# Performance work log

Hardware: AMD Instinct MI355X
Metric: run time of the kernel (lower is better)

The kernel has to match this reference:

```python
import jax, jax.numpy as jnp
import numpy as np

INPUT_DIM = 512
DIM = 512
N_ACTIONS = 128
BATCH = 2048
SEQ = 128
GN_EPS = 1e-5


def setup_inputs() -> dict:
    key = jax.random.key(0)
    ks = jax.random.split(key, 8)
    precondition = jax.random.normal(ks[0], (BATCH, SEQ, INPUT_DIM), dtype=jnp.float32)
    effect = jax.random.normal(ks[1], (BATCH, SEQ, INPUT_DIM), dtype=jnp.float32)
    action = jax.random.randint(ks[2], (BATCH,), 0, N_ACTIONS)
    # learned params (kaiming-ish scales)
    w_scale = 1.0 / np.sqrt(INPUT_DIM)
    W = jax.random.uniform(ks[3], (N_ACTIONS, DIM, DIM), jnp.float32, -1.0/np.sqrt(DIM), 1.0/np.sqrt(DIM))
    pw = jax.random.uniform(ks[4], (DIM, INPUT_DIM), jnp.float32, -w_scale, w_scale)
    pb = jnp.zeros((DIM,), jnp.float32)
    ew = jax.random.uniform(ks[5], (DIM, INPUT_DIM), jnp.float32, -w_scale, w_scale)
    eb = jnp.zeros((DIM,), jnp.float32)
    gamma = jnp.ones((1,), jnp.float32)
    beta = jnp.zeros((1,), jnp.float32)
    return {"precondition": precondition, "effect": effect, "action": action,
            "W": W, "pw": pw, "pb": pb, "ew": ew, "eb": eb,
            "gamma": gamma, "beta": beta}


def _masked_mean(x):
    # sum over seq divided by per-feature nonzero count: [B,S,F] -> [B,F]
    return x.sum(1) / (x != 0).sum(1).astype(x.dtype)


def _group_norm_1_1(x, gamma, beta):
    # GroupNorm(1,1) on [B,1,F]: normalize each sample over its F features
    m = x.mean(-1, keepdims=True)
    v = ((x - m) ** 2).mean(-1, keepdims=True)
    return gamma[0] * (x - m) * jax.lax.rsqrt(v + GN_EPS) + beta[0]


def reference(precondition, effect, action, W, pw, pb, ew, eb, gamma, beta):
    p_avg = _group_norm_1_1(_masked_mean(precondition), gamma, beta)
    e_avg = _group_norm_1_1(_masked_mean(effect), gamma, beta)
    p_embed = p_avg @ pw.T + pb          # [B, DIM]
    e_embed = e_avg @ ew.T + eb          # [B, DIM]
    # (dropouts are identity in eval mode)
    selected = W[action]                 # gather: [B, DIM, DIM]
    p_transformed = jnp.einsum('bij,bj->bi', selected, p_embed)
    return p_transformed, e_embed
```

## Files before the change

kernel.cpp:

```cpp
#include <hip/hip_runtime.h>

#define BATCH 2048
#define SEQ 128
#define F 512
#define NACT 128
#define GN_EPS 1e-5f

__global__ __launch_bounds__(512) void k_avg_gn(const float* __restrict__ pre,
                                                const float* __restrict__ eff,
                                                const float* __restrict__ gamma,
                                                const float* __restrict__ beta,
                                                float* __restrict__ Np,
                                                float* __restrict__ Ne) {
    const int b = blockIdx.x;
    const int t = blockIdx.y;
    const float* x = (t == 0 ? pre : eff) + (size_t)b * SEQ * F;
    float* dst = (t == 0 ? Np : Ne) + (size_t)b * F;

    __shared__ float psum[4][F];
    __shared__ float pcnt[4][F];
    __shared__ float red[8];
    __shared__ float mv[2];

    const int tid = threadIdx.x;
    const int g = tid >> 7;
    const int fb = (tid & 127) << 2;

    float4 s4 = make_float4(0.f, 0.f, 0.f, 0.f);
    float4 c4 = make_float4(0.f, 0.f, 0.f, 0.f);
    for (int s = g; s < SEQ; s += 4) {
        const float4 v = *reinterpret_cast<const float4*>(x + (size_t)s * F + fb);
        s4.x += v.x; s4.y += v.y; s4.z += v.z; s4.w += v.w;
        c4.x += (v.x != 0.f) ? 1.f : 0.f;
        c4.y += (v.y != 0.f) ? 1.f : 0.f;
        c4.z += (v.z != 0.f) ? 1.f : 0.f;
        c4.w += (v.w != 0.f) ? 1.f : 0.f;
    }
    *reinterpret_cast<float4*>(&psum[g][fb]) = s4;
    *reinterpret_cast<float4*>(&pcnt[g][fb]) = c4;
    __syncthreads();

    const int f = tid;
    float sum = psum[0][f] + psum[1][f] + psum[2][f] + psum[3][f];
    float cnt = pcnt[0][f] + pcnt[1][f] + pcnt[2][f] + pcnt[3][f];
    const float avg = sum / cnt;

    const int lane = tid & 63, wv = tid >> 6;

    float r = avg;
    #pragma unroll
    for (int off = 32; off; off >>= 1) r += __shfl_down(r, off, 64);
    if (lane == 0) red[wv] = r;
    __syncthreads();
    if (tid == 0) {
        float m = 0.f;
        #pragma unroll
        for (int i = 0; i < 8; ++i) m += red[i];
        mv[0] = m * (1.f / F);
    }
    __syncthreads();
    const float m = mv[0];
    const float d = avg - m;

    r = d * d;
    #pragma unroll
    for (int off = 32; off; off >>= 1) r += __shfl_down(r, off, 64);
    if (lane == 0) red[wv] = r;
    __syncthreads();
    if (tid == 0) {
        float v = 0.f;
        #pragma unroll
        for (int i = 0; i < 8; ++i) v += red[i];
        mv[1] = v * (1.f / F);
    }
    __syncthreads();
    const float var = mv[1];
    const float inv = 1.f / sqrtf(var + GN_EPS);

    dst[f] = gamma[0] * d * inv + beta[0];
}

__global__ __launch_bounds__(256) void k_sort(const int* __restrict__ action,
                                              int* __restrict__ sorted,
                                              int* __restrict__ gstart) {
    __shared__ int cnt[NACT];
    __shared__ int start[NACT + 1];
    const int tid = threadIdx.x;
    if (tid < NACT) cnt[tid] = 0;
    __syncthreads();
    for (int b = tid; b < BATCH; b += 256) atomicAdd(&cnt[action[b]], 1);
    __syncthreads();
    if (tid == 0) {
        int acc = 0;
        for (int a = 0; a < NACT; ++a) { start[a] = acc; acc += cnt[a]; }
        start[NACT] = acc;
    }
    __syncthreads();
    if (tid <= NACT) gstart[tid] = start[tid];
    if (tid < NACT) cnt[tid] = start[tid];
    __syncthreads();
    for (int b = tid; b < BATCH; b += 256) {
        const int pos = atomicAdd(&cnt[action[b]], 1);
        sorted[pos] = b;
    }
}

__global__ __launch_bounds__(256) void k_embed(const float* __restrict__ Np,
                                               const float* __restrict__ Ne,
                                               const float* __restrict__ pw,
                                               const float* __restrict__ pb,
                                               const float* __restrict__ ew,
                                               const float* __restrict__ eb,
                                               float* __restrict__ Ep,
                                               float* __restrict__ outE) {
    const int z = blockIdx.z;
    const float* A = z ? Ne : Np;
    const float* Bw = z ? ew : pw;
    const float* bias = z ? eb : pb;
    float* D = z ? outE : Ep;

    const int m0 = blockIdx.x * 64;
    const int n0 = blockIdx.y * 64;

    __shared__ float As[16][68];
    __shared__ float Bs[16][68];

    const int tid = threadIdx.x;
    const int lr = tid >> 2;
    const int lk = (tid & 3) << 2;
    const int tx = tid & 15, ty = tid >> 4;

    float acc[4][4] = {};
    for (int k0 = 0; k0 < F; k0 += 16) {
        const float4 av = *reinterpret_cast<const float4*>(A + (size_t)(m0 + lr) * F + k0 + lk);
        const float4 bv = *reinterpret_cast<const float4*>(Bw + (size_t)(n0 + lr) * F + k0 + lk);
        As[lk + 0][lr] = av.x; As[lk + 1][lr] = av.y; As[lk + 2][lr] = av.z; As[lk + 3][lr] = av.w;
        Bs[lk + 0][lr] = bv.x; Bs[lk + 1][lr] = bv.y; Bs[lk + 2][lr] = bv.z; Bs[lk + 3][lr] = bv.w;
        __syncthreads();
        #pragma unroll
        for (int k = 0; k < 16; ++k) {
            const float4 a = *reinterpret_cast<const float4*>(&As[k][ty * 4]);
            const float4 bq = *reinterpret_cast<const float4*>(&Bs[k][tx * 4]);
            acc[0][0] = fmaf(a.x, bq.x, acc[0][0]); acc[0][1] = fmaf(a.x, bq.y, acc[0][1]);
            acc[0][2] = fmaf(a.x, bq.z, acc[0][2]); acc[0][3] = fmaf(a.x, bq.w, acc[0][3]);
            acc[1][0] = fmaf(a.y, bq.x, acc[1][0]); acc[1][1] = fmaf(a.y, bq.y, acc[1][1]);
            acc[1][2] = fmaf(a.y, bq.z, acc[1][2]); acc[1][3] = fmaf(a.y, bq.w, acc[1][3]);
            acc[2][0] = fmaf(a.z, bq.x, acc[2][0]); acc[2][1] = fmaf(a.z, bq.y, acc[2][1]);
            acc[2][2] = fmaf(a.z, bq.z, acc[2][2]); acc[2][3] = fmaf(a.z, bq.w, acc[2][3]);
            acc[3][0] = fmaf(a.w, bq.x, acc[3][0]); acc[3][1] = fmaf(a.w, bq.y, acc[3][1]);
            acc[3][2] = fmaf(a.w, bq.z, acc[3][2]); acc[3][3] = fmaf(a.w, bq.w, acc[3][3]);
        }
        __syncthreads();
    }

    const float4 b4 = *reinterpret_cast<const float4*>(bias + n0 + tx * 4);
    #pragma unroll
    for (int i = 0; i < 4; ++i) {
        float4 o;
        o.x = acc[i][0] + b4.x;
        o.y = acc[i][1] + b4.y;
        o.z = acc[i][2] + b4.z;
        o.w = acc[i][3] + b4.w;
        *reinterpret_cast<float4*>(D + (size_t)(m0 + ty * 4 + i) * F + n0 + tx * 4) = o;
    }
}

__global__ __launch_bounds__(256) void k_transform(const float* __restrict__ W,
                                                   const float* __restrict__ Ep,
                                                   const int* __restrict__ sorted,
                                                   const int* __restrict__ gstart,
                                                   float* __restrict__ outP) {
    const int a = blockIdx.x;
    const int s0 = gstart[a], s1 = gstart[a + 1];
    if (s0 == s1) return;

    const int rowbase = blockIdx.y * 128 + (threadIdx.x >> 6) * 32;
    const int lane = threadIdx.x & 63;
    const float* Wa = W + (size_t)a * F * F;

    for (int c0 = s0; c0 < s1; c0 += 8) {
        int bb[8];
        float4 e0[8], e1[8];
        #pragma unroll
        for (int q = 0; q < 8; ++q) {
            const int src = (c0 + q < s1) ? (c0 + q) : s0;
            bb[q] = sorted[src];
            const float* er = Ep + (size_t)bb[q] * F + lane * 8;
            e0[q] = *reinterpret_cast<const float4*>(er);
            e1[q] = *reinterpret_cast<const float4*>(er + 4);
        }
        for (int r = 0; r < 32; ++r) {
            const int i = rowbase + r;
            const float* wr = Wa + (size_t)i * F + lane * 8;
            const float4 w0 = *reinterpret_cast<const float4*>(wr);
            const float4 w1 = *reinterpret_cast<const float4*>(wr + 4);
            float p[8];
            #pragma unroll
            for (int q = 0; q < 8; ++q) {
                float s = w0.x * e0[q].x;
                s = fmaf(w0.y, e0[q].y, s);
                s = fmaf(w0.z, e0[q].z, s);
                s = fmaf(w0.w, e0[q].w, s);
                s = fmaf(w1.x, e1[q].x, s);
                s = fmaf(w1.y, e1[q].y, s);
                s = fmaf(w1.z, e1[q].z, s);
                s = fmaf(w1.w, e1[q].w, s);
                p[q] = s;
            }
            #pragma unroll
            for (int q = 0; q < 8; ++q) {
                #pragma unroll
                for (int off = 32; off; off >>= 1) p[q] += __shfl_down(p[q], off, 64);
            }
            if (lane == 0) {
                #pragma unroll
                for (int q = 0; q < 8; ++q)
                    if (c0 + q < s1) outP[(size_t)bb[q] * F + i] = p[q];
            }
        }
    }
}

extern "C" void kernel_launch(void* const* d_in, const int* in_sizes, int n_in,
                              void* d_out, int out_size, void* d_ws, size_t ws_size,
                              hipStream_t stream) {
    const float* pre    = (const float*)d_in[0];
    const float* eff    = (const float*)d_in[1];
    const int*   action = (const int*)d_in[2];
    const float* W      = (const float*)d_in[3];
    const float* pw     = (const float*)d_in[4];
    const float* pb     = (const float*)d_in[5];
    const float* ew     = (const float*)d_in[6];
    const float* eb     = (const float*)d_in[7];
    const float* gamma  = (const float*)d_in[8];
    const float* beta   = (const float*)d_in[9];

    float* out  = (float*)d_out;
    float* outP = out;
    float* outE = out + (size_t)BATCH * F;

    float* Np = (float*)d_ws;
    float* Ne = Np + (size_t)BATCH * F;
    float* Ep = Ne + (size_t)BATCH * F;
    int* sorted = (int*)(Ep + (size_t)BATCH * F);
    int* gstart = sorted + BATCH;

    k_avg_gn<<<dim3(BATCH, 2), 512, 0, stream>>>(pre, eff, gamma, beta, Np, Ne);
    k_sort<<<1, 256, 0, stream>>>(action, sorted, gstart);
    k_embed<<<dim3(2048 / 64, 512 / 64, 2), 256, 0, stream>>>(Np, Ne, pw, pb, ew, eb, Ep, outE);
    k_transform<<<dim3(NACT, 4), 256, 0, stream>>>(W, Ep, sorted, gstart, outP);
}
```

Before: 1.238 ms.

## Fuse averaging, group norm, embedding GEMV and sort into one kernel

Merges the masked-mean/group-norm kernel, the action counting-sort kernel and the tiled embedding GEMM into a single launch. Each block now normalizes its row into shared memory and immediately computes the embedding as a per-thread dot product against pw/ew, and one extra block does the sort. This drops two launches and the round trip of the normalized intermediates through global memory. The trade-off is that the embedding becomes a GEMV per row that rereads the full 512x512 weight matrix in every block, relying on L2 to absorb it. The transform kernel is also split into twice as many row blocks to raise parallelism.

```diff
diff --git a/kernel.cpp b/kernel.cpp
--- a/kernel.cpp
+++ b/kernel.cpp
@@ -6,23 +6,58 @@
 #define NACT 128
 #define GN_EPS 1e-5f
 
-__global__ __launch_bounds__(512) void k_avg_gn(const float* __restrict__ pre,
-                                                const float* __restrict__ eff,
-                                                const float* __restrict__ gamma,
-                                                const float* __restrict__ beta,
-                                                float* __restrict__ Np,
-                                                float* __restrict__ Ne) {
-    const int b = blockIdx.x;
-    const int t = blockIdx.y;
+__global__ __launch_bounds__(512) void k_fused(const float* __restrict__ pre,
+                                               const float* __restrict__ eff,
+                                               const int* __restrict__ action,
+                                               const float* __restrict__ pw,
+                                               const float* __restrict__ pb,
+                                               const float* __restrict__ ew,
+                                               const float* __restrict__ eb,
+                                               const float* __restrict__ gamma,
+                                               const float* __restrict__ beta,
+                                               float* __restrict__ Ep,
+                                               float* __restrict__ outE,
+                                               int* __restrict__ sorted,
+                                               int* __restrict__ gstart) {
+    const int blk = blockIdx.x;
+    const int tid = threadIdx.x;
+
+    if (blk == 2 * BATCH) {
+        __shared__ int cnt[NACT];
+        __shared__ int start[NACT + 1];
+        if (tid < NACT) cnt[tid] = 0;
+        __syncthreads();
+        for (int b = tid; b < BATCH; b += 512) atomicAdd(&cnt[action[b]], 1);
+        __syncthreads();
+        if (tid == 0) {
+            int acc = 0;
+            for (int a = 0; a < NACT; ++a) { start[a] = acc; acc += cnt[a]; }
+            start[NACT] = acc;
+        }
+        __syncthreads();
+        if (tid <= NACT) gstart[tid] = start[tid];
+        if (tid < NACT) cnt[tid] = start[tid];
+        __syncthreads();
+        for (int b = tid; b < BATCH; b += 512) {
+            const int pos = atomicAdd(&cnt[action[b]], 1);
+            sorted[pos] = b;
+        }
+        return;
+    }
+
+    const int b = blk >> 1;
+    const int t = blk & 1;
     const float* x = (t == 0 ? pre : eff) + (size_t)b * SEQ * F;
-    float* dst = (t == 0 ? Np : Ne) + (size_t)b * F;
+    const float* wmat = t == 0 ? pw : ew;
+    const float* bias = t == 0 ? pb : eb;
+    float* dst = (t == 0 ? Ep : outE) + (size_t)b * F;
 
     __shared__ float psum[4][F];
     __shared__ float pcnt[4][F];
+    __shared__ float nvec[F];
     __shared__ float red[8];
     __shared__ float mv[2];
 
-    const int tid = threadIdx.x;
     const int g = tid >> 7;
     const int fb = (tid & 127) << 2;
 
@@ -41,9 +76,9 @@
     __syncthreads();
 
     const int f = tid;
-    float sum = psum[0][f] + psum[1][f] + psum[2][f] + psum[3][f];
-    float cnt = pcnt[0][f] + pcnt[1][f] + pcnt[2][f] + pcnt[3][f];
-    const float avg = sum / cnt;
+    const float sum = psum[0][f] + psum[1][f] + psum[2][f] + psum[3][f];
+    const float cntf = pcnt[0][f] + pcnt[1][f] + pcnt[2][f] + pcnt[3][f];
+    const float avg = sum / cntf;
 
     const int lane = tid & 63, wv = tid >> 6;
 
@@ -74,95 +109,25 @@
         mv[1] = v * (1.f / F);
     }
     __syncthreads();
-    const float var = mv[1];
-    const float inv = 1.f / sqrtf(var + GN_EPS);
-
-    dst[f] = gamma[0] * d * inv + beta[0];
-}
-
-__global__ __launch_bounds__(256) void k_sort(const int* __restrict__ action,
-                                              int* __restrict__ sorted,
-                                              int* __restrict__ gstart) {
-    __shared__ int cnt[NACT];
-    __shared__ int start[NACT + 1];
-    const int tid = threadIdx.x;
-    if (tid < NACT) cnt[tid] = 0;
-    __syncthreads();
-    for (int b = tid; b < BATCH; b += 256) atomicAdd(&cnt[action[b]], 1);
-    __syncthreads();
-    if (tid == 0) {
-        int acc = 0;
-        for (int a = 0; a < NACT; ++a) { start[a] = acc; acc += cnt[a]; }
-        start[NACT] = acc;
-    }
-    __syncthreads();
-    if (tid <= NACT) gstart[tid] = start[tid];
-    if (tid < NACT) cnt[tid] = start[tid];
-    __syncthreads();
-    for (int b = tid; b < BATCH; b += 256) {
-        const int pos = atomicAdd(&cnt[action[b]], 1);
-        sorted[pos] = b;
-    }
-}
-
-__global__ __launch_bounds__(256) void k_embed(const float* __restrict__ Np,
-                                               const float* __restrict__ Ne,
-                                               const float* __restrict__ pw,
-                                               const float* __restrict__ pb,
-                                               const float* __restrict__ ew,
-                                               const float* __restrict__ eb,
-                                               float* __restrict__ Ep,
-                                               float* __restrict__ outE) {
-    const int z = blockIdx.z;
-    const float* A = z ? Ne : Np;
-    const float* Bw = z ? ew : pw;
-    const float* bias = z ? eb : pb;
-    float* D = z ? outE : Ep;
-
-    const int m0 = blockIdx.x * 64;
-    const int n0 = blockIdx.y * 64;
-
-    __shared__ float As[16][68];
-    __shared__ float Bs[16][68];
-
-    const int tid = threadIdx.x;
-    const int lr = tid >> 2;
-    const int lk = (tid & 3) << 2;
-    const int tx = tid & 15, ty = tid >> 4;
-
-    float acc[4][4] = {};
-    for (int k0 = 0; k0 < F; k0 += 16) {
-        const float4 av = *reinterpret_cast<const float4*>(A + (size_t)(m0 + lr) * F + k0 + lk);
-        const float4 bv = *reinterpret_cast<const float4*>(Bw + (size_t)(n0 + lr) * F + k0 + lk);
-        As[lk + 0][lr] = av.x; As[lk + 1][lr] = av.y; As[lk + 2][lr] = av.z; As[lk + 3][lr] = av.w;
-        Bs[lk + 0][lr] = bv.x; Bs[lk + 1][lr] = bv.y; Bs[lk + 2][lr] = bv.z; Bs[lk + 3][lr] = bv.w;
-        __syncthreads();
-        #pragma unroll
-        for (int k = 0; k < 16; ++k) {
-            const float4 a = *reinterpret_cast<const float4*>(&As[k][ty * 4]);
-            const float4 bq = *reinterpret_cast<const float4*>(&Bs[k][tx * 4]);
-            acc[0][0] = fmaf(a.x, bq.x, acc[0][0]); acc[0][1] = fmaf(a.x, bq.y, acc[0][1]);
-            acc[0][2] = fmaf(a.x, bq.z, acc[0][2]); acc[0][3] = fmaf(a.x, bq.w, acc[0][3]);
-            acc[1][0] = fmaf(a.y, bq.x, acc[1][0]); acc[1][1] = fmaf(a.y, bq.y, acc[1][1]);
-            acc[1][2] = fmaf(a.y, bq.z, acc[1][2]); acc[1][3] = fmaf(a.y, bq.w, acc[1][3]);
-            acc[2][0] = fmaf(a.z, bq.x, acc[2][0]); acc[2][1] = fmaf(a.z, bq.y, acc[2][1]);
-            acc[2][2] = fmaf(a.z, bq.z, acc[2][2]); acc[2][3] = fmaf(a.z, bq.w, acc[2][3]);
-            acc[3][0] = fmaf(a.w, bq.x, acc[3][0]); acc[3][1] = fmaf(a.w, bq.y, acc[3][1]);
-            acc[3][2] = fmaf(a.w, bq.z, acc[3][2]); acc[3][3] = fmaf(a.w, bq.w, acc[3][3]);
-        }
-        __syncthreads();
-    }
-
-    const float4 b4 = *reinterpret_cast<const float4*>(bias + n0 + tx * 4);
-    #pragma unroll
-    for (int i = 0; i < 4; ++i) {
-        float4 o;
-        o.x = acc[i][0] + b4.x;
-        o.y = acc[i][1] + b4.y;
-        o.z = acc[i][2] + b4.z;
-        o.w = acc[i][3] + b4.w;
-        *reinterpret_cast<float4*>(D + (size_t)(m0 + ty * 4 + i) * F + n0 + tx * 4) = o;
-    }
+    const float inv = 1.f / sqrtf(mv[1] + GN_EPS);
+
+    nvec[f] = gamma[0] * d * inv + beta[0];
+    __syncthreads();
+
+    const float* wr = wmat + (size_t)f * F;
+    float acc0 = 0.f, acc1 = 0.f;
+    #pragma unroll 4
+    for (int k = 0; k < F; k += 8) {
+        const float4 w0 = *reinterpret_cast<const float4*>(wr + k);
+        const float4 w1 = *reinterpret_cast<const float4*>(wr + k + 4);
+        const float4 n0 = *reinterpret_cast<const float4*>(&nvec[k]);
+        const float4 n1 = *reinterpret_cast<const float4*>(&nvec[k + 4]);
+        acc0 = fmaf(w0.x, n0.x, acc0); acc0 = fmaf(w0.y, n0.y, acc0);
+        acc0 = fmaf(w0.z, n0.z, acc0); acc0 = fmaf(w0.w, n0.w, acc0);
+        acc1 = fmaf(w1.x, n1.x, acc1); acc1 = fmaf(w1.y, n1.y, acc1);
+        acc1 = fmaf(w1.z, n1.z, acc1); acc1 = fmaf(w1.w, n1.w, acc1);
+    }
+    dst[f] = acc0 + acc1 + bias[f];
 }
 
 __global__ __launch_bounds__(256) void k_transform(const float* __restrict__ W,
@@ -174,7 +139,7 @@
     const int s0 = gstart[a], s1 = gstart[a + 1];
     if (s0 == s1) return;
 
-    const int rowbase = blockIdx.y * 128 + (threadIdx.x >> 6) * 32;
+    const int rowbase = blockIdx.y * 64 + (threadIdx.x >> 6) * 16;
     const int lane = threadIdx.x & 63;
     const float* Wa = W + (size_t)a * F * F;
 
@@ -189,7 +154,7 @@
             e0[q] = *reinterpret_cast<const float4*>(er);
             e1[q] = *reinterpret_cast<const float4*>(er + 4);
         }
-        for (int r = 0; r < 32; ++r) {
+        for (int r = 0; r < 16; ++r) {
             const int i = rowbase + r;
             const float* wr = Wa + (size_t)i * F + lane * 8;
             const float4 w0 = *reinterpret_cast<const float4*>(wr);
@@ -239,14 +204,11 @@
     float* outP = out;
     float* outE = out + (size_t)BATCH * F;
 
-    float* Np = (float*)d_ws;
-    float* Ne = Np + (size_t)BATCH * F;
-    float* Ep = Ne + (size_t)BATCH * F;
+    float* Ep = (float*)d_ws;
     int* sorted = (int*)(Ep + (size_t)BATCH * F);
     int* gstart = sorted + BATCH;
 
-    k_avg_gn<<<dim3(BATCH, 2), 512, 0, stream>>>(pre, eff, gamma, beta, Np, Ne);
-    k_sort<<<1, 256, 0, stream>>>(action, sorted, gstart);
-    k_embed<<<dim3(2048 / 64, 512 / 64, 2), 256, 0, stream>>>(Np, Ne, pw, pb, ew, eb, Ep, outE);
-    k_transform<<<dim3(NACT, 4), 256, 0, stream>>>(W, Ep, sorted, gstart, outP);
+    k_fused<<<2 * BATCH + 1, 512, 0, stream>>>(pre, eff, action, pw, pb, ew, eb,
+                                               gamma, beta, Ep, outE, sorted, gstart);
+    k_transform<<<dim3(NACT, 8), 256, 0, stream>>>(W, Ep, sorted, gstart, outP);
 }
```

Result: slower. 1.598 ms (+29.1%).
